# Performance work log

Hardware: AMD Instinct MI355X
Metric: run time of the kernel (lower is better)

The kernel has to match this reference:

```python
import jax, jax.numpy as jnp
import numpy as np


def _qrnn_forward(X, W, b):
    seq_len, batch, d = X.shape
    H = W.shape[0] // 3
    Y = jnp.einsum('sbd,hd->sbh', X, W) + b  # [S,B,3H]
    Z, F, O = jnp.split(Y, 3, axis=2)
    Z = jnp.tanh(Z)
    F = jax.nn.sigmoid(F)

    # ForgetMult with hidden_init=None: h_0 = f_0*z_0; h_t = f_t*z_t + (1-f_t)*h_{t-1}
    # Equivalent to scan from h_{-1} = 0.
    def step(h_prev, fz):
        f_t, z_t = fz
        h = f_t * z_t + (1.0 - f_t) * h_prev
        return h, h

    h0 = jnp.zeros((batch, H), dtype=X.dtype)
    _, C = jax.lax.scan(step, h0, (F, Z))  # [S,B,H]
    Hout = jax.nn.sigmoid(O) * C
    return Hout, C[-1:, :, :]


def setup_inputs() -> dict:
    key = jax.random.key(0)
    k1, k2, k3 = jax.random.split(key, 3)
    S, B, D, Hdim = 1024, 16, 1024, 1024
    X = jax.random.normal(k1, (S, B, D), dtype=jnp.float32)
    W = jax.random.normal(k2, (3 * Hdim, D), dtype=jnp.float32) * (1.0 / np.sqrt(D))
    b = jax.random.normal(k3, (3 * Hdim,), dtype=jnp.float32) * 0.01
    return {"X": X, "W": W, "b": b}


def reference(X, W, b):
    return _qrnn_forward(X, W, b)
```

## Files before the change

kernel.cpp:

```cpp
#include <hip/hip_runtime.h>
#include <hip/hip_bf16.h>
#include <stdint.h>

typedef __bf16 bf16x8 __attribute__((ext_vector_type(8)));
typedef __bf16 bf16x4 __attribute__((ext_vector_type(4)));
typedef float f32x4 __attribute__((ext_vector_type(4)));

constexpr int S = 1024, Bsz = 16, Hd = 1024;
constexpr int M = S * Bsz;
constexpr int N = 3 * Hd;
constexpr int K = 1024;
constexpr int BM = 128, BN = 128, BK = 64;
constexpr int NCH = 32, CS = S / NCH;
constexpr int BH = Bsz * Hd;
constexpr int NX8 = 2097152;
constexpr int NW8 = 393216;

__device__ __forceinline__ float fast_sigmoid(float x) { return 1.0f / (1.0f + __expf(-x)); }
__device__ __forceinline__ float fast_tanh(float x) { return 2.0f / (1.0f + __expf(-2.0f * x)) - 1.0f; }

__device__ __forceinline__ void gld_lds16(const __bf16* g, __bf16* l) {
  __builtin_amdgcn_global_load_lds(
      (const __attribute__((address_space(1))) void*)g,
      (__attribute__((address_space(3))) void*)l,
      16, 0, 0);
}

__global__ void convert_all(const float* __restrict__ X, const float* __restrict__ W,
                            __bf16* __restrict__ Xb, __bf16* __restrict__ Wb) {
  int i = blockIdx.x * 256 + threadIdx.x;
  const float* s;
  __bf16* d;
  int idx;
  if (i < NX8) { s = X; d = Xb; idx = i; }
  else if (i < NX8 + NW8) { s = W; d = Wb; idx = i - NX8; }
  else return;
  const float4* s4 = (const float4*)s;
  float4 a = s4[2 * idx], b = s4[2 * idx + 1];
  bf16x8 v;
  v[0] = (__bf16)a.x; v[1] = (__bf16)a.y; v[2] = (__bf16)a.z; v[3] = (__bf16)a.w;
  v[4] = (__bf16)b.x; v[5] = (__bf16)b.y; v[6] = (__bf16)b.z; v[7] = (__bf16)b.w;
  *((bf16x8*)d + idx) = v;
}

__global__ __launch_bounds__(256) void gemm_act(const __bf16* __restrict__ A,
                                                const __bf16* __restrict__ Bw,
                                                const float* __restrict__ bias,
                                                __bf16* __restrict__ Y) {
  __shared__ __align__(16) __bf16 As[BM * BK];
  __shared__ __align__(16) __bf16 Bs[BN * BK];
  const int t = threadIdx.x;
  const int lane = t & 63;
  const int wave = t >> 6;
  const int wm = wave >> 1, wn = wave & 1;
  const int tn = blockIdx.x % (N / BN);
  const int tm = blockIdx.x / (N / BN);
  const int m0 = tm * BM, n0 = tn * BN;
  const int lrow = lane & 15;
  const int quad = lane >> 4;

  const int srow = t >> 3;
  const int scw = t & 7;
  const __bf16* gA[4];
  const __bf16* gB[4];
  __bf16* lA[4];
  __bf16* lB[4];
#pragma unroll
  for (int i = 0; i < 4; ++i) {
    gA[i] = A + (size_t)(m0 + srow + i * 32) * K + scw * 8;
    gB[i] = Bw + (size_t)(n0 + srow + i * 32) * K + scw * 8;
    lA[i] = As + i * 2048 + wave * 512;
    lB[i] = Bs + i * 2048 + wave * 512;
  }

  f32x4 acc[4][4] = {};

  for (int k0 = 0; k0 < K; k0 += BK) {
    __syncthreads();
#pragma unroll
    for (int i = 0; i < 4; ++i) {
      gld_lds16(gA[i], lA[i]);
      gld_lds16(gB[i], lB[i]);
    }
#pragma unroll
    for (int i = 0; i < 4; ++i) { gA[i] += BK; gB[i] += BK; }
    __syncthreads();

#pragma unroll
    for (int s = 0; s < 2; ++s) {
      bf16x8 af[4], bfr[4];
#pragma unroll
      for (int mi = 0; mi < 4; ++mi)
        af[mi] = *(const bf16x8*)(&As[(wm * 64 + mi * 16 + lrow) * BK + s * 32 + quad * 8]);
#pragma unroll
      for (int ni = 0; ni < 4; ++ni)
        bfr[ni] = *(const bf16x8*)(&Bs[(wn * 64 + ni * 16 + lrow) * BK + s * 32 + quad * 8]);
#pragma unroll
      for (int mi = 0; mi < 4; ++mi)
#pragma unroll
        for (int ni = 0; ni < 4; ++ni)
          acc[mi][ni] = __builtin_amdgcn_mfma_f32_16x16x32_bf16(af[mi], bfr[ni], acc[mi][ni], 0, 0, 0);
    }
  }

#pragma unroll
  for (int ni = 0; ni < 4; ++ni) {
    int col = n0 + wn * 64 + ni * 16 + lrow;
    float bv = bias[col];
    bool is_tanh = (col < Hd);
#pragma unroll
    for (int mi = 0; mi < 4; ++mi) {
#pragma unroll
      for (int r = 0; r < 4; ++r) {
        int m = m0 + wm * 64 + mi * 16 + quad * 4 + r;
        float y = acc[mi][ni][r] + bv;
        float v = is_tanh ? fast_tanh(y) : fast_sigmoid(y);
        Y[(size_t)m * N + col] = (__bf16)v;
      }
    }
  }
}

__global__ __launch_bounds__(256) void scan_pass1(const __bf16* __restrict__ Y,
                                                  float* __restrict__ Ac,
                                                  float* __restrict__ Bc) {
  int tid = blockIdx.x * 256 + threadIdx.x;
  int c = tid >> 12;
  int bh4 = tid & 4095;
  int b = bh4 >> 8, h0 = (bh4 & 255) * 4;
  const size_t sstep = (size_t)Bsz * N;
  const __bf16* base = Y + (size_t)(c * CS) * sstep + (size_t)b * N + h0;
  float A[4], Bv[4];
#pragma unroll
  for (int l = 0; l < 4; ++l) { A[l] = 1.0f; Bv[l] = 0.0f; }
  for (int j0 = 0; j0 < CS; j0 += 8) {
    bf16x4 z[8], f[8];
#pragma unroll
    for (int j = 0; j < 8; ++j) {
      const __bf16* p = base + (size_t)(j0 + j) * sstep;
      z[j] = *(const bf16x4*)p;
      f[j] = *(const bf16x4*)(p + Hd);
    }
#pragma unroll
    for (int j = 0; j < 8; ++j)
#pragma unroll
      for (int l = 0; l < 4; ++l) {
        float ff = (float)f[j][l];
        float a = 1.0f - ff;
        Bv[l] = fmaf(a, Bv[l], ff * (float)z[j][l]);
        A[l] *= a;
      }
  }
  int ob = c * BH + b * Hd + h0;
#pragma unroll
  for (int l = 0; l < 4; ++l) { Ac[ob + l] = A[l]; Bc[ob + l] = Bv[l]; }
}

__global__ __launch_bounds__(256) void scan_pass2(const float* __restrict__ Ac,
                                                  const float* __restrict__ Bc,
                                                  float* __restrict__ hin,
                                                  float* __restrict__ clast) {
  int bh = blockIdx.x * 256 + threadIdx.x;
  float h = 0.0f;
#pragma unroll 4
  for (int c = 0; c < NCH; ++c) {
    hin[c * BH + bh] = h;
    h = fmaf(Ac[c * BH + bh], h, Bc[c * BH + bh]);
  }
  clast[bh] = h;
}

__global__ __launch_bounds__(256) void scan_pass3(const __bf16* __restrict__ Y,
                                                  const float* __restrict__ hin,
                                                  float* __restrict__ hout) {
  int tid = blockIdx.x * 256 + threadIdx.x;
  int c = tid >> 12;
  int bh4 = tid & 4095;
  int b = bh4 >> 8, h0 = (bh4 & 255) * 4;
  const size_t sstep = (size_t)Bsz * N;
  const __bf16* base = Y + (size_t)(c * CS) * sstep + (size_t)b * N + h0;
  float* ob = hout + (size_t)(c * CS) * BH + (size_t)b * Hd + h0;
  float hp[4];
  int hb = c * BH + b * Hd + h0;
#pragma unroll
  for (int l = 0; l < 4; ++l) hp[l] = hin[hb + l];
  for (int j0 = 0; j0 < CS; j0 += 4) {
    bf16x4 z[4], f[4], o[4];
#pragma unroll
    for (int j = 0; j < 4; ++j) {
      const __bf16* p = base + (size_t)(j0 + j) * sstep;
      z[j] = *(const bf16x4*)p;
      f[j] = *(const bf16x4*)(p + Hd);
      o[j] = *(const bf16x4*)(p + 2 * Hd);
    }
#pragma unroll
    for (int j = 0; j < 4; ++j) {
      float out4[4];
#pragma unroll
      for (int l = 0; l < 4; ++l) {
        float ff = (float)f[j][l];
        hp[l] = fmaf(ff, (float)z[j][l] - hp[l], hp[l]);
        out4[l] = (float)o[j][l] * hp[l];
      }
      *(float4*)(ob + (size_t)(j0 + j) * BH) = make_float4(out4[0], out4[1], out4[2], out4[3]);
    }
  }
}

extern "C" void kernel_launch(void* const* d_in, const int* in_sizes, int n_in,
                              void* d_out, int out_size, void* d_ws, size_t ws_size,
                              hipStream_t stream) {
  const float* X = (const float*)d_in[0];
  const float* W = (const float*)d_in[1];
  const float* bias = (const float*)d_in[2];
  float* out = (float*)d_out;

  char* ws = (char*)d_ws;
  __bf16* Xb = (__bf16*)ws;
  __bf16* Wb = (__bf16*)(ws + 33554432);
  __bf16* Yv = (__bf16*)(ws + 39845888);
  float* Ac = (float*)(ws + 39845888 + 100663296);
  float* Bc = Ac + NCH * BH;
  float* hin = Bc + NCH * BH;

  convert_all<<<(NX8 + NW8) / 256, 256, 0, stream>>>(X, W, Xb, Wb);

  dim3 ggrid((M / BM) * (N / BN));
  dim3 sgrid(NCH * BH / 4 / 256);
  gemm_act<<<ggrid, 256, 0, stream>>>(Xb, Wb, bias, Yv);
  scan_pass1<<<sgrid, 256, 0, stream>>>(Yv, Ac, Bc);
  scan_pass2<<<BH / 256, 256, 0, stream>>>(Ac, Bc, hin, out + 16777216);
  scan_pass3<<<sgrid, 256, 0, stream>>>(Yv, hin, out);
}
```

Before: 333.9 us.

## Switch GEMM to 32x32x16 MFMA with swizzled LDS and smaller K tile

Replaces the 16x16x32 bf16 MFMA tiling with 32x32x16 MFMA (2x2 tiles per wave), halves the K tile to 32, and adds an XOR swizzle to the LDS layout for both stores and fragment reads. The aim is fewer MFMA issues and fewer LDS bank conflicts per unit of work. The cost is twice as many K iterations, each with two barriers and a smaller load batch, which may expose more global-to-LDS latency.

```diff
diff --git a/kernel.cpp b/kernel.cpp
--- a/kernel.cpp
+++ b/kernel.cpp
@@ -5,12 +5,13 @@
 typedef __bf16 bf16x8 __attribute__((ext_vector_type(8)));
 typedef __bf16 bf16x4 __attribute__((ext_vector_type(4)));
 typedef float f32x4 __attribute__((ext_vector_type(4)));
+typedef float f32x16 __attribute__((ext_vector_type(16)));
 
 constexpr int S = 1024, Bsz = 16, Hd = 1024;
 constexpr int M = S * Bsz;
 constexpr int N = 3 * Hd;
 constexpr int K = 1024;
-constexpr int BM = 128, BN = 128, BK = 64;
+constexpr int BM = 128, BN = 128, BK = 32;
 constexpr int NCH = 32, CS = S / NCH;
 constexpr int BH = Bsz * Hd;
 constexpr int NX8 = 2097152;
@@ -56,64 +57,63 @@
   const int tn = blockIdx.x % (N / BN);
   const int tm = blockIdx.x / (N / BN);
   const int m0 = tm * BM, n0 = tn * BN;
-  const int lrow = lane & 15;
-  const int quad = lane >> 4;
-
-  const int srow = t >> 3;
-  const int scw = t & 7;
-  const __bf16* gA[4];
-  const __bf16* gB[4];
-  __bf16* lA[4];
-  __bf16* lB[4];
-#pragma unroll
-  for (int i = 0; i < 4; ++i) {
-    gA[i] = A + (size_t)(m0 + srow + i * 32) * K + scw * 8;
-    gB[i] = Bw + (size_t)(n0 + srow + i * 32) * K + scw * 8;
-    lA[i] = As + i * 2048 + wave * 512;
-    lB[i] = Bs + i * 2048 + wave * 512;
-  }
-
-  f32x4 acc[4][4] = {};
+  const int l32 = lane & 31;
+  const int khalf = lane >> 5;
+
+  const int srow = t >> 2;
+  const int sswz = (srow >> 1) & 3;
+  const int cw_log = (t & 3) ^ sswz;
+  const __bf16* gA0 = A + (size_t)(m0 + srow) * K + cw_log * 8;
+  const __bf16* gA1 = gA0 + (size_t)64 * K;
+  const __bf16* gB0 = Bw + (size_t)(n0 + srow) * K + cw_log * 8;
+  const __bf16* gB1 = gB0 + (size_t)64 * K;
+  __bf16* lA0 = As + wave * 512;
+  __bf16* lA1 = As + 2048 + wave * 512;
+  __bf16* lB0 = Bs + wave * 512;
+  __bf16* lB1 = Bs + 2048 + wave * 512;
+
+  const int rswz = (l32 >> 1) & 3;
+
+  f32x16 acc[2][2] = {};
 
   for (int k0 = 0; k0 < K; k0 += BK) {
     __syncthreads();
-#pragma unroll
-    for (int i = 0; i < 4; ++i) {
-      gld_lds16(gA[i], lA[i]);
-      gld_lds16(gB[i], lB[i]);
-    }
-#pragma unroll
-    for (int i = 0; i < 4; ++i) { gA[i] += BK; gB[i] += BK; }
+    gld_lds16(gA0, lA0);
+    gld_lds16(gA1, lA1);
+    gld_lds16(gB0, lB0);
+    gld_lds16(gB1, lB1);
+    gA0 += BK; gA1 += BK; gB0 += BK; gB1 += BK;
     __syncthreads();
 
 #pragma unroll
     for (int s = 0; s < 2; ++s) {
-      bf16x8 af[4], bfr[4];
-#pragma unroll
-      for (int mi = 0; mi < 4; ++mi)
-        af[mi] = *(const bf16x8*)(&As[(wm * 64 + mi * 16 + lrow) * BK + s * 32 + quad * 8]);
-#pragma unroll
-      for (int ni = 0; ni < 4; ++ni)
-        bfr[ni] = *(const bf16x8*)(&Bs[(wn * 64 + ni * 16 + lrow) * BK + s * 32 + quad * 8]);
-#pragma unroll
-      for (int mi = 0; mi < 4; ++mi)
-#pragma unroll
-        for (int ni = 0; ni < 4; ++ni)
-          acc[mi][ni] = __builtin_amdgcn_mfma_f32_16x16x32_bf16(af[mi], bfr[ni], acc[mi][ni], 0, 0, 0);
-    }
-  }
-
-#pragma unroll
-  for (int ni = 0; ni < 4; ++ni) {
-    int col = n0 + wn * 64 + ni * 16 + lrow;
+      const int p = (s * 2 + khalf) ^ rswz;
+      bf16x8 af[2], bfr[2];
+#pragma unroll
+      for (int mi = 0; mi < 2; ++mi)
+        af[mi] = *(const bf16x8*)(&As[(wm * 64 + mi * 32 + l32) * BK + p * 8]);
+#pragma unroll
+      for (int ni = 0; ni < 2; ++ni)
+        bfr[ni] = *(const bf16x8*)(&Bs[(wn * 64 + ni * 32 + l32) * BK + p * 8]);
+#pragma unroll
+      for (int mi = 0; mi < 2; ++mi)
+#pragma unroll
+        for (int ni = 0; ni < 2; ++ni)
+          acc[mi][ni] = __builtin_amdgcn_mfma_f32_32x32x16_bf16(af[mi], bfr[ni], acc[mi][ni], 0, 0, 0);
+    }
+  }
+
+#pragma unroll
+  for (int ni = 0; ni < 2; ++ni) {
+    int col = n0 + wn * 64 + ni * 32 + l32;
     float bv = bias[col];
     bool is_tanh = (col < Hd);
 #pragma unroll
-    for (int mi = 0; mi < 4; ++mi) {
-#pragma unroll
-      for (int r = 0; r < 4; ++r) {
-        int m = m0 + wm * 64 + mi * 16 + quad * 4 + r;
-        float y = acc[mi][ni][r] + bv;
+    for (int mi = 0; mi < 2; ++mi) {
+#pragma unroll
+      for (int reg = 0; reg < 16; ++reg) {
+        int m = m0 + wm * 64 + mi * 32 + (reg & 3) + 8 * (reg >> 2) + 4 * khalf;
+        float y = acc[mi][ni][reg] + bv;
         float v = is_tanh ? fast_tanh(y) : fast_sigmoid(y);
         Y[(size_t)m * N + col] = (__bf16)v;
       }
```

After: 326.6 us. 1.02x faster.
